# Performance work log

Hardware: AMD Instinct MI355X
Metric: run time of the kernel (lower is better)

The kernel has to match this reference:

```python
import jax, jax.numpy as jnp
import numpy as np

B, L, N, H = 512, 50, 16, 128
NUM_USERS = NUM_ITEMS = 100000


def setup_inputs() -> dict:
    key = jax.random.key(0)
    ks = jax.random.split(key, 20)
    s = lambda i, shape: jax.random.normal(ks[i], shape, dtype=jnp.float32) * 0.05
    return {
        "user_ids": jax.random.randint(ks[0], (B,), 0, NUM_USERS),
        "item_ids": jax.random.randint(ks[1], (B,), 0, NUM_ITEMS),
        "history": jax.random.randint(ks[2], (B, L), 0, NUM_ITEMS),
        "neighbor_emb": jax.random.normal(ks[3], (B, L, N, H), dtype=jnp.float32),
        "user_table": s(4, (NUM_USERS, H)),
        "item_table": s(5, (NUM_ITEMS, H)),
        "Wa": s(6, (2 * H, 96)), "ba": jnp.zeros((96,), jnp.float32),
        "W1": s(7, (96, 48)), "b1": jnp.zeros((48,), jnp.float32),
        "W2": s(8, (48, 16)), "b2": jnp.zeros((16,), jnp.float32),
        "W3": s(9, (16, 1)), "b3": jnp.zeros((1,), jnp.float32),
        # 4 heads of Linear(H, H//4) concatenated on the output dim == one [H, H] GEMM
        "Wmh": s(10, (H, H)), "bmh": jnp.zeros((H,), jnp.float32),
        "Wfc1": s(11, (2 * H, H)), "bfc1": jnp.zeros((H,), jnp.float32),
        "Wout": s(12, (H, 1)), "bout": jnp.zeros((1,), jnp.float32),
    }


def reference(user_ids, item_ids, history, neighbor_emb,
              user_table, item_table, Wa, ba, W1, b1, W2, b2, W3, b3,
              Wmh, bmh, Wfc1, bfc1, Wout, bout):
    user_emb = user_table[user_ids]                      # [B, H]
    item_emb = item_table[item_ids]                      # computed but unused (as in original)
    hist_emb = item_table[history]                       # [B, L, H]

    # concat(history broadcast over neighbors, neighbor_emb) -> [B, L, N, 2H]
    hist_b = jnp.broadcast_to(hist_emb[:, :, None, :], (B, L, N, H))
    att_in = jnp.concatenate([hist_b, neighbor_emb], axis=-1)

    scores = jax.nn.relu(att_in @ Wa + ba)               # [B, L, N, 96]
    h1 = jax.nn.relu(scores @ W1 + b1)                   # [B, L, N, 48]
    h2 = jax.nn.relu(h1 @ W2 + b2)                       # [B, L, N, 16]
    logits = (h2 @ W3 + b3)[..., 0]                      # [B, L, N]
    attn = jax.nn.softmax(logits, axis=-1)               # softmax over neighbor dim

    agg = jnp.einsum('bln,blnh->blh', attn, neighbor_emb)  # [B, L, H]
    mh = agg @ Wmh + bmh                                 # fused multihead projections
    pooled = mh.mean(axis=1)                             # [B, H]

    comb = jnp.concatenate([user_emb, pooled], axis=-1)  # [B, 2H]
    hidden = jax.nn.relu(comb @ Wfc1 + bfc1)             # dropout is identity in eval
    out = jax.nn.sigmoid(hidden @ Wout + bout)[:, 0]     # [B]
    return out
```

## Files before the change

kernel.cpp:

```cpp
#include <hip/hip_runtime.h>

constexpr int B  = 512, L = 50, N = 16, H = 128;
constexpr int C1 = 96, C2 = 48, C3 = 16;

typedef __bf16  bf16x8 __attribute__((ext_vector_type(8)));
typedef float   f32x4  __attribute__((ext_vector_type(4)));
typedef unsigned u32x4 __attribute__((ext_vector_type(4)));

constexpr int OFF_HS = 0;
constexpr int OFF_SC = 1536;
constexpr int OFF_H1 = 3200;
constexpr int PW_SIZE   = 4352;
constexpr int SC_STRIDE = 104;
constexpr int H1_STRIDE = 72;

__device__ __forceinline__ bf16x8 cvt8(float4 a, float4 b) {
  bf16x8 r;
  r[0] = (__bf16)a.x; r[1] = (__bf16)a.y; r[2] = (__bf16)a.z; r[3] = (__bf16)a.w;
  r[4] = (__bf16)b.x; r[5] = (__bf16)b.y; r[6] = (__bf16)b.z; r[7] = (__bf16)b.w;
  return r;
}
__device__ __forceinline__ float bf16lo(unsigned u) { return __uint_as_float(u << 16); }
__device__ __forceinline__ float bf16hi(unsigned u) { return __uint_as_float(u & 0xffff0000u); }

__global__ __launch_bounds__(512, 2) void fused_kernel(
    const int*   __restrict__ user_ids,
    const int*   __restrict__ history,
    const float* __restrict__ neighbor_emb,
    const float* __restrict__ user_table,
    const float* __restrict__ item_table,
    const float* __restrict__ Wa,  const float* __restrict__ ba,
    const float* __restrict__ W1,  const float* __restrict__ b1,
    const float* __restrict__ W2,  const float* __restrict__ b2,
    const float* __restrict__ W3,
    const float* __restrict__ Wmh,  const float* __restrict__ bmh,
    const float* __restrict__ Wfc1, const float* __restrict__ bfc1,
    const float* __restrict__ Wout, const float* __restrict__ bout,
    float* __restrict__ out)
{
  __shared__ __align__(16) __bf16 sWa[48 * 64 * 8];
  __shared__ __align__(16) __bf16 sW1[9 * 64 * 8];
  __shared__ __align__(16) __bf16 sPW[8][PW_SIZE];
  __shared__ float sRed[8][128];
  __shared__ float sAgg2[2][128];
  __shared__ float sComb[2][2 * H];
  __shared__ float sP[8];

  const int tid  = threadIdx.x;
  const int wave = tid >> 6;
  const int lane = tid & 63;
  const int g    = lane >> 4;
  const int c    = lane & 15;

  for (int e = tid; e < 48 * 64; e += 512) {
    int lv = e & 63, frag = e >> 6;
    int s = frag & 7, t = frag >> 3;
    int k0 = s * 32 + ((lv >> 4) << 3);
    int cc = t * 16 + (lv & 15);
    bf16x8 v;
    #pragma unroll
    for (int j = 0; j < 8; ++j) v[j] = (__bf16)Wa[(k0 + j) * C1 + cc];
    *(bf16x8*)&sWa[e * 8] = v;
  }
  for (int e = tid; e < 9 * 64; e += 512) {
    int lv = e & 63, frag = e >> 6;
    int s = frag % 3, t = frag / 3;
    int k0 = s * 32 + ((lv >> 4) << 3);
    int cc = t * 16 + (lv & 15);
    bf16x8 v;
    #pragma unroll
    for (int j = 0; j < 8; ++j) v[j] = (__bf16)W1[(k0 + j) * C2 + cc];
    *(bf16x8*)&sW1[e * 8] = v;
  }
  for (int i = tid; i < 8 * (16 * H1_STRIDE / 2); i += 512) {
    int w = i / (16 * H1_STRIDE / 2), r = i % (16 * H1_STRIDE / 2);
    ((unsigned*)&sPW[w][OFF_H1])[r] = 0u;
  }

  float ba_r[6], b1_r[3];
  #pragma unroll
  for (int t = 0; t < 6; ++t) ba_r[t] = ba[t * 16 + c];
  #pragma unroll
  for (int t = 0; t < 3; ++t) b1_r[t] = b1[t * 16 + c];
  const float b2_r = b2[c];
  const float w3_r = W3[c];
  bf16x8 w2f[2];
  #pragma unroll
  for (int s = 0; s < 2; ++s)
    #pragma unroll
    for (int j = 0; j < 8; ++j) {
      int k = s * 32 + g * 8 + j;
      w2f[s][j] = (k < C2) ? (__bf16)W2[k * C3 + c] : (__bf16)0.f;
    }

  __syncthreads();

  const int bb = blockIdx.x * 2 + (wave >> 2);
  const int wl = wave & 3;
  __bf16* PW = sPW[wave];
  const int nIter = (L - wl + 3) / 4;

  {
    int li  = wl + 4 * c;
    int idx = (li < L) ? history[bb * L + li] : history[bb * L];
    const float* hr = item_table + (size_t)idx * H;
    f32x4 acch[6];
    #pragma unroll
    for (int t = 0; t < 6; ++t) acch[t] = (f32x4){0.f, 0.f, 0.f, 0.f};
    #pragma unroll
    for (int s = 0; s < 4; ++s) {
      const float* p = hr + s * 32 + g * 8;
      bf16x8 a = cvt8(*(const float4*)p, *(const float4*)(p + 4));
      #pragma unroll
      for (int t = 0; t < 6; ++t)
        acch[t] = __builtin_amdgcn_mfma_f32_16x16x32_bf16(
            a, *(const bf16x8*)&sWa[((t * 8 + s) * 64 + lane) * 8], acch[t], 0, 0, 0);
    }
    #pragma unroll
    for (int t = 0; t < 6; ++t)
      #pragma unroll
      for (int r = 0; r < 4; ++r)
        PW[OFF_HS + (4 * g + r) * 96 + t * 16 + c] = (__bf16)(acch[t][r] + ba_r[t]);
  }

  const float* nb0 = neighbor_emb + (size_t)(bb * L + wl) * (N * H) + c * H + g * 8;
  float4 nf[8];
  {
    const float* p = nb0;
    #pragma unroll
    for (int s = 0; s < 4; ++s) {
      nf[2 * s]     = *(const float4*)(p + s * 32);
      nf[2 * s + 1] = *(const float4*)(p + s * 32 + 4);
    }
  }
  float aggp[32];
  #pragma unroll
  for (int i = 0; i < 32; ++i) aggp[i] = 0.f;

  for (int it = 0; it < nIter; ++it) {
    bf16x8 aA[4];
    #pragma unroll
    for (int s = 0; s < 4; ++s) aA[s] = cvt8(nf[2 * s], nf[2 * s + 1]);
    if (it + 1 < nIter) {
      const float* p = nb0 + (size_t)(it + 1) * (4 * N * H);
      #pragma unroll
      for (int s = 0; s < 4; ++s) {
        nf[2 * s]     = *(const float4*)(p + s * 32);
        nf[2 * s + 1] = *(const float4*)(p + s * 32 + 4);
      }
    }

    f32x4 acc[6];
    #pragma unroll
    for (int t = 0; t < 6; ++t) acc[t] = (f32x4){0.f, 0.f, 0.f, 0.f};
    #pragma unroll
    for (int s = 0; s < 4; ++s)
      #pragma unroll
      for (int t = 0; t < 6; ++t)
        acc[t] = __builtin_amdgcn_mfma_f32_16x16x32_bf16(
            aA[s], *(const bf16x8*)&sWa[((t * 8 + 4 + s) * 64 + lane) * 8], acc[t], 0, 0, 0);
    float hs[6];
    #pragma unroll
    for (int t = 0; t < 6; ++t) hs[t] = (float)PW[OFF_HS + it * 96 + t * 16 + c];
    #pragma unroll
    for (int t = 0; t < 6; ++t)
      #pragma unroll
      for (int r = 0; r < 4; ++r)
        PW[OFF_SC + (4 * g + r) * SC_STRIDE + t * 16 + c] =
            (__bf16)fmaxf(acc[t][r] + hs[t], 0.f);

    f32x4 acc2[3];
    #pragma unroll
    for (int t = 0; t < 3; ++t) acc2[t] = (f32x4){0.f, 0.f, 0.f, 0.f};
    #pragma unroll
    for (int s = 0; s < 3; ++s) {
      bf16x8 a2 = *(const bf16x8*)&PW[OFF_SC + c * SC_STRIDE + s * 32 + g * 8];
      #pragma unroll
      for (int t = 0; t < 3; ++t)
        acc2[t] = __builtin_amdgcn_mfma_f32_16x16x32_bf16(
            a2, *(const bf16x8*)&sW1[((t * 3 + s) * 64 + lane) * 8], acc2[t], 0, 0, 0);
    }
    #pragma unroll
    for (int t = 0; t < 3; ++t)
      #pragma unroll
      for (int r = 0; r < 4; ++r)
        PW[OFF_H1 + (4 * g + r) * H1_STRIDE + t * 16 + c] =
            (__bf16)fmaxf(acc2[t][r] + b1_r[t], 0.f);

    f32x4 acc3 = (f32x4){0.f, 0.f, 0.f, 0.f};
    #pragma unroll
    for (int s = 0; s < 2; ++s) {
      bf16x8 a3 = *(const bf16x8*)&PW[OFF_H1 + c * H1_STRIDE + s * 32 + g * 8];
      acc3 = __builtin_amdgcn_mfma_f32_16x16x32_bf16(a3, w2f[s], acc3, 0, 0, 0);
    }

    float lp[4];
    #pragma unroll
    for (int r = 0; r < 4; ++r) lp[r] = fmaxf(acc3[r] + b2_r, 0.f) * w3_r;
    #pragma unroll
    for (int off = 1; off < 16; off <<= 1) {
      lp[0] += __shfl_xor(lp[0], off);
      lp[1] += __shfl_xor(lp[1], off);
      lp[2] += __shfl_xor(lp[2], off);
      lp[3] += __shfl_xor(lp[3], off);
    }
    float m = fmaxf(fmaxf(lp[0], lp[1]), fmaxf(lp[2], lp[3]));
    m = fmaxf(m, __shfl_xor(m, 16));
    m = fmaxf(m, __shfl_xor(m, 32));
    float e0 = __expf(lp[0] - m), e1 = __expf(lp[1] - m);
    float e2 = __expf(lp[2] - m), e3 = __expf(lp[3] - m);
    float ss = e0 + e1 + e2 + e3;
    ss += __shfl_xor(ss, 16);
    ss += __shfl_xor(ss, 32);
    const float rs = 1.f / ss;

    const int src = (c >> 2) << 4;
    float t0 = __shfl(e0, src), t1 = __shfl(e1, src);
    float t2 = __shfl(e2, src), t3 = __shfl(e3, src);
    float s01 = (c & 1) ? t1 : t0;
    float s23 = (c & 1) ? t3 : t2;
    const float w = ((c & 2) ? s23 : s01) * rs;

    #pragma unroll
    for (int s = 0; s < 4; ++s) {
      u32x4 au = __builtin_bit_cast(u32x4, aA[s]);
      #pragma unroll
      for (int q = 0; q < 4; ++q) {
        unsigned u = au[q];
        aggp[s * 8 + 2 * q]     = fmaf(w, bf16lo(u), aggp[s * 8 + 2 * q]);
        aggp[s * 8 + 2 * q + 1] = fmaf(w, bf16hi(u), aggp[s * 8 + 2 * q + 1]);
      }
    }
  }

  #pragma unroll
  for (int off = 1; off < 16; off <<= 1)
    #pragma unroll
    for (int i = 0; i < 32; ++i) aggp[i] += __shfl_xor(aggp[i], off);
  if (c == 0) {
    #pragma unroll
    for (int s = 0; s < 4; ++s) {
      float4 v0 = {aggp[8 * s + 0], aggp[8 * s + 1], aggp[8 * s + 2], aggp[8 * s + 3]};
      float4 v1 = {aggp[8 * s + 4], aggp[8 * s + 5], aggp[8 * s + 6], aggp[8 * s + 7]};
      *(float4*)&sRed[wave][32 * s + 8 * g]     = v0;
      *(float4*)&sRed[wave][32 * s + 8 * g + 4] = v1;
    }
  }
  __syncthreads();

  const int bs  = tid >> 8;
  const int t2  = tid & 255;
  const int bb2 = blockIdx.x * 2 + bs;
  if (t2 < 128) {
    float s = 0.f;
    #pragma unroll
    for (int w = 0; w < 4; ++w) s += sRed[bs * 4 + w][t2];
    sAgg2[bs][t2] = s * (1.0f / L);
    sComb[bs][t2] = user_table[(size_t)user_ids[bb2] * H + t2];
  }
  __syncthreads();
  if (t2 < 128) {
    float p = bmh[t2];
    #pragma unroll 8
    for (int k = 0; k < H; ++k) p = fmaf(sAgg2[bs][k], Wmh[k * H + t2], p);
    sComb[bs][H + t2] = p;
  }
  __syncthreads();
  float partial = 0.f;
  if (t2 < 128) {
    float hd = bfc1[t2];
    #pragma unroll 8
    for (int k = 0; k < 2 * H; ++k) hd = fmaf(sComb[bs][k], Wfc1[k * H + t2], hd);
    hd = fmaxf(hd, 0.f);
    partial = hd * Wout[t2];
  }
  #pragma unroll
  for (int off = 32; off > 0; off >>= 1) partial += __shfl_down(partial, off);
  if (lane == 0) sP[wave] = partial;
  __syncthreads();
  if (tid < 2) {
    float s = sP[tid * 4] + sP[tid * 4 + 1] + bout[0];
    out[blockIdx.x * 2 + tid] = 1.f / (1.f + __expf(-s));
  }
}

extern "C" void kernel_launch(void* const* d_in, const int* in_sizes, int n_in,
                              void* d_out, int out_size, void* d_ws, size_t ws_size,
                              hipStream_t stream) {
  const int*   user_ids     = (const int*)  d_in[0];
  const int*   history      = (const int*)  d_in[2];
  const float* neighbor_emb = (const float*)d_in[3];
  const float* user_table   = (const float*)d_in[4];
  const float* item_table   = (const float*)d_in[5];
  const float* Wa   = (const float*)d_in[6];
  const float* ba   = (const float*)d_in[7];
  const float* W1   = (const float*)d_in[8];
  const float* b1   = (const float*)d_in[9];
  const float* W2   = (const float*)d_in[10];
  const float* b2   = (const float*)d_in[11];
  const float* W3   = (const float*)d_in[12];
  const float* Wmh  = (const float*)d_in[14];
  const float* bmh  = (const float*)d_in[15];
  const float* Wfc1 = (const float*)d_in[16];
  const float* bfc1 = (const float*)d_in[17];
  const float* Wout = (const float*)d_in[18];
  const float* bout = (const float*)d_in[19];

  float* out = (float*)d_out;

  hipLaunchKernelGGL(fused_kernel, dim3(B / 2), dim3(512), 0, stream,
                     user_ids, history, neighbor_emb, user_table, item_table,
                     Wa, ba, W1, b1, W2, b2, W3,
                     Wmh, bmh, Wfc1, bfc1, Wout, bout, out);
}
```

Before: 67.88 us.

## Keep MLP activations in registers via transposed MFMA and cross-lane shuffles

Swaps the MFMA operand order so each wave computes transposed outputs. Intermediate scores and hidden activations are packed to bf16 in registers and redistributed with ds_bpermute shuffles instead of round-tripping through per-wave LDS scratch. Biases are folded into the accumulator initial values, and the logit reduction and softmax are simplified to use fewer shuffles. This trades LDS stores, loads and bank traffic for many more shuffle instructions, and cuts LDS footprint, which could raise occupancy.

```diff
diff --git a/kernel.cpp b/kernel.cpp
--- a/kernel.cpp
+++ b/kernel.cpp
@@ -3,16 +3,9 @@
 constexpr int B  = 512, L = 50, N = 16, H = 128;
 constexpr int C1 = 96, C2 = 48, C3 = 16;
 
-typedef __bf16  bf16x8 __attribute__((ext_vector_type(8)));
-typedef float   f32x4  __attribute__((ext_vector_type(4)));
-typedef unsigned u32x4 __attribute__((ext_vector_type(4)));
-
-constexpr int OFF_HS = 0;
-constexpr int OFF_SC = 1536;
-constexpr int OFF_H1 = 3200;
-constexpr int PW_SIZE   = 4352;
-constexpr int SC_STRIDE = 104;
-constexpr int H1_STRIDE = 72;
+typedef __bf16   bf16x8 __attribute__((ext_vector_type(8)));
+typedef float    f32x4  __attribute__((ext_vector_type(4)));
+typedef unsigned u32x4  __attribute__((ext_vector_type(4)));
 
 __device__ __forceinline__ bf16x8 cvt8(float4 a, float4 b) {
   bf16x8 r;
@@ -22,6 +15,11 @@
 }
 __device__ __forceinline__ float bf16lo(unsigned u) { return __uint_as_float(u << 16); }
 __device__ __forceinline__ float bf16hi(unsigned u) { return __uint_as_float(u & 0xffff0000u); }
+__device__ __forceinline__ unsigned pkbf(float lo, float hi) {
+  unsigned r;
+  asm("v_cvt_pk_bf16_f32 %0, %1, %2" : "=v"(r) : "v"(lo), "v"(hi));
+  return r;
+}
 
 __global__ __launch_bounds__(512, 2) void fused_kernel(
     const int*   __restrict__ user_ids,
@@ -40,7 +38,7 @@
 {
   __shared__ __align__(16) __bf16 sWa[48 * 64 * 8];
   __shared__ __align__(16) __bf16 sW1[9 * 64 * 8];
-  __shared__ __align__(16) __bf16 sPW[8][PW_SIZE];
+  __shared__ __align__(16) __bf16 sHS[8][16 * C1];
   __shared__ float sRed[8][128];
   __shared__ float sAgg2[2][128];
   __shared__ float sComb[2][2 * H];
@@ -72,18 +70,12 @@
     for (int j = 0; j < 8; ++j) v[j] = (__bf16)W1[(k0 + j) * C2 + cc];
     *(bf16x8*)&sW1[e * 8] = v;
   }
-  for (int i = tid; i < 8 * (16 * H1_STRIDE / 2); i += 512) {
-    int w = i / (16 * H1_STRIDE / 2), r = i % (16 * H1_STRIDE / 2);
-    ((unsigned*)&sPW[w][OFF_H1])[r] = 0u;
-  }
-
-  float ba_r[6], b1_r[3];
-  #pragma unroll
-  for (int t = 0; t < 6; ++t) ba_r[t] = ba[t * 16 + c];
-  #pragma unroll
-  for (int t = 0; t < 3; ++t) b1_r[t] = b1[t * 16 + c];
-  const float b2_r = b2[c];
-  const float w3_r = W3[c];
+
+  const f32x4 b1v0 = *(const f32x4*)&b1[ 0 + 4 * g];
+  const f32x4 b1v1 = *(const f32x4*)&b1[16 + 4 * g];
+  const f32x4 b1v2 = *(const f32x4*)&b1[32 + 4 * g];
+  const f32x4 b2v  = *(const f32x4*)&b2[4 * g];
+  const f32x4 w3v  = *(const f32x4*)&W3[4 * g];
   bf16x8 w2f[2];
   #pragma unroll
   for (int s = 0; s < 2; ++s)
@@ -97,10 +89,13 @@
 
   const int bb = blockIdx.x * 2 + (wave >> 2);
   const int wl = wave & 3;
-  __bf16* PW = sPW[wave];
+  __bf16* HS = sHS[wave];
   const int nIter = (L - wl + 3) / 4;
 
   {
+    float ba_r[6];
+    #pragma unroll
+    for (int t = 0; t < 6; ++t) ba_r[t] = ba[t * 16 + c];
     int li  = wl + 4 * c;
     int idx = (li < L) ? history[bb * L + li] : history[bb * L];
     const float* hr = item_table + (size_t)idx * H;
@@ -120,7 +115,7 @@
     for (int t = 0; t < 6; ++t)
       #pragma unroll
       for (int r = 0; r < 4; ++r)
-        PW[OFF_HS + (4 * g + r) * 96 + t * 16 + c] = (__bf16)(acch[t][r] + ba_r[t]);
+        HS[(4 * g + r) * C1 + t * 16 + c] = (__bf16)(acch[t][r] + ba_r[t]);
   }
 
   const float* nb0 = neighbor_emb + (size_t)(bb * L + wl) * (N * H) + c * H + g * 8;
@@ -137,6 +132,10 @@
   #pragma unroll
   for (int i = 0; i < 32; ++i) aggp[i] = 0.f;
 
+  const int  src_lo = ((g & 1) << 5) | c;
+  const int  src_hi = src_lo + 16;
+  const bool gh     = (g >> 1) & 1;
+
   for (int it = 0; it < nIter; ++it) {
     bf16x8 aA[4];
     #pragma unroll
@@ -152,74 +151,91 @@
 
     f32x4 acc[6];
     #pragma unroll
-    for (int t = 0; t < 6; ++t) acc[t] = (f32x4){0.f, 0.f, 0.f, 0.f};
+    for (int t = 0; t < 6; ++t) {
+      uint2 hw = *(const uint2*)&HS[it * C1 + 16 * t + 4 * g];
+      acc[t][0] = bf16lo(hw.x); acc[t][1] = bf16hi(hw.x);
+      acc[t][2] = bf16lo(hw.y); acc[t][3] = bf16hi(hw.y);
+    }
     #pragma unroll
     for (int s = 0; s < 4; ++s)
       #pragma unroll
       for (int t = 0; t < 6; ++t)
         acc[t] = __builtin_amdgcn_mfma_f32_16x16x32_bf16(
-            aA[s], *(const bf16x8*)&sWa[((t * 8 + 4 + s) * 64 + lane) * 8], acc[t], 0, 0, 0);
-    float hs[6];
-    #pragma unroll
-    for (int t = 0; t < 6; ++t) hs[t] = (float)PW[OFF_HS + it * 96 + t * 16 + c];
-    #pragma unroll
-    for (int t = 0; t < 6; ++t)
-      #pragma unroll
-      for (int r = 0; r < 4; ++r)
-        PW[OFF_SC + (4 * g + r) * SC_STRIDE + t * 16 + c] =
-            (__bf16)fmaxf(acc[t][r] + hs[t], 0.f);
-
-    f32x4 acc2[3];
-    #pragma unroll
-    for (int t = 0; t < 3; ++t) acc2[t] = (f32x4){0.f, 0.f, 0.f, 0.f};
+            *(const bf16x8*)&sWa[((t * 8 + 4 + s) * 64 + lane) * 8], aA[s],
+            acc[t], 0, 0, 0);
+    unsigned pku[6][2];
+    #pragma unroll
+    for (int t = 0; t < 6; ++t) {
+      pku[t][0] = pkbf(fmaxf(acc[t][0], 0.f), fmaxf(acc[t][1], 0.f));
+      pku[t][1] = pkbf(fmaxf(acc[t][2], 0.f), fmaxf(acc[t][3], 0.f));
+    }
+
+    f32x4 acc2[3] = {b1v0, b1v1, b1v2};
     #pragma unroll
     for (int s = 0; s < 3; ++s) {
-      bf16x8 a2 = *(const bf16x8*)&PW[OFF_SC + c * SC_STRIDE + s * 32 + g * 8];
-      #pragma unroll
-      for (int t = 0; t < 3; ++t)
-        acc2[t] = __builtin_amdgcn_mfma_f32_16x16x32_bf16(
-            a2, *(const bf16x8*)&sW1[((t * 3 + s) * 64 + lane) * 8], acc2[t], 0, 0, 0);
-    }
-    #pragma unroll
-    for (int t = 0; t < 3; ++t)
-      #pragma unroll
-      for (int r = 0; r < 4; ++r)
-        PW[OFF_H1 + (4 * g + r) * H1_STRIDE + t * 16 + c] =
-            (__bf16)fmaxf(acc2[t][r] + b1_r[t], 0.f);
-
-    f32x4 acc3 = (f32x4){0.f, 0.f, 0.f, 0.f};
-    #pragma unroll
-    for (int s = 0; s < 2; ++s) {
-      bf16x8 a3 = *(const bf16x8*)&PW[OFF_H1 + c * H1_STRIDE + s * 32 + g * 8];
-      acc3 = __builtin_amdgcn_mfma_f32_16x16x32_bf16(a3, w2f[s], acc3, 0, 0, 0);
-    }
-
-    float lp[4];
-    #pragma unroll
-    for (int r = 0; r < 4; ++r) lp[r] = fmaxf(acc3[r] + b2_r, 0.f) * w3_r;
-    #pragma unroll
-    for (int off = 1; off < 16; off <<= 1) {
-      lp[0] += __shfl_xor(lp[0], off);
-      lp[1] += __shfl_xor(lp[1], off);
-      lp[2] += __shfl_xor(lp[2], off);
-      lp[3] += __shfl_xor(lp[3], off);
-    }
-    float m = fmaxf(fmaxf(lp[0], lp[1]), fmaxf(lp[2], lp[3]));
-    m = fmaxf(m, __shfl_xor(m, 16));
-    m = fmaxf(m, __shfl_xor(m, 32));
-    float e0 = __expf(lp[0] - m), e1 = __expf(lp[1] - m);
-    float e2 = __expf(lp[2] - m), e3 = __expf(lp[3] - m);
-    float ss = e0 + e1 + e2 + e3;
-    ss += __shfl_xor(ss, 16);
-    ss += __shfl_xor(ss, 32);
-    const float rs = 1.f / ss;
-
-    const int src = (c >> 2) << 4;
-    float t0 = __shfl(e0, src), t1 = __shfl(e1, src);
-    float t2 = __shfl(e2, src), t3 = __shfl(e3, src);
-    float s01 = (c & 1) ? t1 : t0;
-    float s23 = (c & 1) ? t3 : t2;
-    const float w = ((c & 2) ? s23 : s01) * rs;
+      unsigned a0 = __shfl((int)pku[2 * s][0], src_lo);
+      unsigned a1 = __shfl((int)pku[2 * s][1], src_lo);
+      unsigned a2 = __shfl((int)pku[2 * s][0], src_hi);
+      unsigned a3 = __shfl((int)pku[2 * s][1], src_hi);
+      unsigned d0 = __shfl((int)pku[2 * s + 1][0], src_lo);
+      unsigned d1 = __shfl((int)pku[2 * s + 1][1], src_lo);
+      unsigned d2 = __shfl((int)pku[2 * s + 1][0], src_hi);
+      unsigned d3 = __shfl((int)pku[2 * s + 1][1], src_hi);
+      u32x4 wv = {gh ? d0 : a0, gh ? d1 : a1, gh ? d2 : a2, gh ? d3 : a3};
+      bf16x8 bf2 = __builtin_bit_cast(bf16x8, wv);
+      #pragma unroll
+      for (int t2 = 0; t2 < 3; ++t2)
+        acc2[t2] = __builtin_amdgcn_mfma_f32_16x16x32_bf16(
+            *(const bf16x8*)&sW1[((t2 * 3 + s) * 64 + lane) * 8], bf2,
+            acc2[t2], 0, 0, 0);
+    }
+    unsigned pk2[3][2];
+    #pragma unroll
+    for (int t2 = 0; t2 < 3; ++t2) {
+      pk2[t2][0] = pkbf(fmaxf(acc2[t2][0], 0.f), fmaxf(acc2[t2][1], 0.f));
+      pk2[t2][1] = pkbf(fmaxf(acc2[t2][2], 0.f), fmaxf(acc2[t2][3], 0.f));
+    }
+
+    f32x4 acc3 = b2v;
+    {
+      unsigned a0 = __shfl((int)pk2[0][0], src_lo);
+      unsigned a1 = __shfl((int)pk2[0][1], src_lo);
+      unsigned a2 = __shfl((int)pk2[0][0], src_hi);
+      unsigned a3 = __shfl((int)pk2[0][1], src_hi);
+      unsigned d0 = __shfl((int)pk2[1][0], src_lo);
+      unsigned d1 = __shfl((int)pk2[1][1], src_lo);
+      unsigned d2 = __shfl((int)pk2[1][0], src_hi);
+      unsigned d3 = __shfl((int)pk2[1][1], src_hi);
+      u32x4 wv = {gh ? d0 : a0, gh ? d1 : a1, gh ? d2 : a2, gh ? d3 : a3};
+      acc3 = __builtin_amdgcn_mfma_f32_16x16x32_bf16(
+          w2f[0], __builtin_bit_cast(bf16x8, wv), acc3, 0, 0, 0);
+      unsigned e0 = __shfl((int)pk2[2][0], src_lo);
+      unsigned e1 = __shfl((int)pk2[2][1], src_lo);
+      unsigned e2 = __shfl((int)pk2[2][0], src_hi);
+      unsigned e3 = __shfl((int)pk2[2][1], src_hi);
+      u32x4 wv2 = {gh ? 0u : e0, gh ? 0u : e1, gh ? 0u : e2, gh ? 0u : e3};
+      acc3 = __builtin_amdgcn_mfma_f32_16x16x32_bf16(
+          w2f[1], __builtin_bit_cast(bf16x8, wv2), acc3, 0, 0, 0);
+    }
+
+    float lg = 0.f;
+    #pragma unroll
+    for (int r = 0; r < 4; ++r) lg = fmaf(fmaxf(acc3[r], 0.f), w3v[r], lg);
+    lg += __shfl_xor(lg, 16);
+    lg += __shfl_xor(lg, 32);
+
+    float mm = lg;
+    mm = fmaxf(mm, __shfl_xor(mm, 1));
+    mm = fmaxf(mm, __shfl_xor(mm, 2));
+    mm = fmaxf(mm, __shfl_xor(mm, 4));
+    mm = fmaxf(mm, __shfl_xor(mm, 8));
+    float e = __expf(lg - mm);
+    float se = e;
+    se += __shfl_xor(se, 1);
+    se += __shfl_xor(se, 2);
+    se += __shfl_xor(se, 4);
+    se += __shfl_xor(se, 8);
+    const float w = e / se;
 
     #pragma unroll
     for (int s = 0; s < 4; ++s) {
```

Result: faster. 66.39 us (-2.2%).
